# Performance work log

Measured on AMD Instinct MI355X. Metric: run time of the kernel, lower is better.

The kernel has to match this reference:

```python
import jax, jax.numpy as jnp
import numpy as np

BATCH, SEQ, D_MODEL, N_HEADS, D_HEAD = 2, 2048, 2048, 16, 128
ATTN_SCALE = np.sqrt(D_HEAD).astype(np.float32)
IGNORE = jnp.float32(-1e5)


def setup_inputs() -> dict:
    key = jax.random.key(0)
    ks = jax.random.split(key, 5)
    init = 1.0 / np.sqrt(D_MODEL)
    return {
        "x": jax.random.normal(ks[0], (BATCH, SEQ, D_MODEL), jnp.float32),
        "W_Q": jax.random.normal(ks[1], (N_HEADS, D_MODEL, D_HEAD), jnp.float32) * init,
        "W_K": jax.random.normal(ks[2], (N_HEADS, D_MODEL, D_HEAD), jnp.float32) * init,
        "W_V": jax.random.normal(ks[3], (N_HEADS, D_MODEL, D_HEAD), jnp.float32) * init,
        "W_O": jax.random.normal(ks[4], (N_HEADS, D_HEAD, D_MODEL), jnp.float32) * init,
        "b_Q": jnp.zeros((N_HEADS, D_HEAD), jnp.float32),
        "b_K": jnp.zeros((N_HEADS, D_HEAD), jnp.float32),
        "b_V": jnp.zeros((N_HEADS, D_HEAD), jnp.float32),
        "b_O": jnp.zeros((D_MODEL,), jnp.float32),
    }


def reference(x, W_Q, W_K, W_V, W_O, b_Q, b_K, b_V, b_O):
    # q,k,v: [batch, pos, head, d_head]
    q = jnp.einsum('bpd,hde->bphe', x, W_Q) + b_Q
    k = jnp.einsum('bpd,hde->bphe', x, W_K) + b_K
    v = jnp.einsum('bpd,hde->bphe', x, W_V) + b_V
    # scores: [batch, head, query_pos, key_pos]
    scores = jnp.einsum('bqhe,bkhe->bhqk', q, k) / ATTN_SCALE
    S = x.shape[1]
    causal = jnp.tril(jnp.ones((S, S), bool))
    scores = jnp.where(causal, scores, IGNORE)
    attn = jax.nn.softmax(scores, axis=-1)
    z = jnp.einsum('bkhe,bhqk->bqhe', v, attn)
    out = jnp.einsum('bqhe,hed->bqd', z, W_O) + b_O
    return out
```

## Files before the change

kernel.cpp:

```cpp
#include <hip/hip_runtime.h>

typedef unsigned int uint;
typedef unsigned short ushort;
typedef __bf16 bf16x8 __attribute__((ext_vector_type(8)));
typedef float f32x4 __attribute__((ext_vector_type(4)));
typedef uint u32x4 __attribute__((ext_vector_type(4)));

#define DEV static __device__ __forceinline__

#define BATCH 2
#define SEQ 2048
#define DMODEL 2048
#define NHEADS 16
#define DHEAD 128
#define MROWS (BATCH*SEQ)
#define RSCALE 0.08838834764831845f

DEV bf16x8 as_frag(u32x4 v) { return __builtin_bit_cast(bf16x8, v); }
DEV ushort f2bf(float f) {
  uint u = __builtin_bit_cast(uint, f);
  u += 0x7fffu + ((u >> 16) & 1u);
  return (ushort)(u >> 16);
}
DEV u32x4 lds_ld16(const ushort* p) { return *(const u32x4*)p; }

DEV void async_cp16(const ushort* g, ushort* l) {
  __builtin_amdgcn_global_load_lds(
      (const __attribute__((address_space(1))) uint*)g,
      (__attribute__((address_space(3))) uint*)l, 16, 0, 0);
}

__global__ __launch_bounds__(256) void convert_f32_bf16(
    const float* __restrict__ src, ushort* __restrict__ dst, int n4)
{
  int i = blockIdx.x * 256 + threadIdx.x;
  if (i >= n4) return;
  const float4* s4 = (const float4*)src;
  float4 v = s4[i];
  union { ushort u[4]; uint2 w; } o;
  o.u[0] = f2bf(v.x); o.u[1] = f2bf(v.y); o.u[2] = f2bf(v.z); o.u[3] = f2bf(v.w);
  ((uint2*)dst)[i] = o.w;
}

__global__ __launch_bounds__(256) void transpose_f32_bf16(
    const float* __restrict__ src, ushort* __restrict__ dst, int R, int C)
{
  __shared__ ushort t[32][33];
  size_t slice = (size_t)blockIdx.z * R * C;
  src += slice; dst += slice;
  int c0 = blockIdx.x * 32, r0 = blockIdx.y * 32;
  int x = threadIdx.x & 31, y = threadIdx.x >> 5;
  #pragma unroll
  for (int i = 0; i < 32; i += 8)
    t[y + i][x] = f2bf(src[(size_t)(r0 + y + i) * C + (c0 + x)]);
  __syncthreads();
  #pragma unroll
  for (int i = 0; i < 32; i += 8)
    dst[(size_t)(c0 + y + i) * R + (r0 + x)] = t[x][y + i];
}

__global__ __launch_bounds__(256, 3) void gemm_qkv(
    const ushort* __restrict__ xb,
    const ushort* __restrict__ WqT, const ushort* __restrict__ WkT,
    const ushort* __restrict__ WvT,
    const float* __restrict__ bQ, const float* __restrict__ bK,
    const float* __restrict__ bV,
    ushort* __restrict__ Qo, ushort* __restrict__ Ko, ushort* __restrict__ Vt)
{
  int mt = blockIdx.x;
  int h  = blockIdx.y;
  int which = blockIdx.z;
  const ushort* Bt = (which == 0) ? WqT : (which == 1) ? WkT : WvT;
  const float* bias = (which == 0) ? bQ : (which == 1) ? bK : bV;
  Bt += (size_t)h * DHEAD * DMODEL;
  bias += h * DHEAD;

  __shared__ __align__(16) ushort As[128 * 64];
  __shared__ __align__(16) ushort Bs[128 * 64];

  int tid = threadIdx.x, lane = tid & 63, w = tid >> 6;
  int wm = w >> 1, wn = w & 1;
  int l16 = lane & 15, quad = lane >> 4;

  const ushort* Ag = xb + (size_t)(mt * 128) * DMODEL;

  int soff[4]; int sc[4];
  #pragma unroll
  for (int t = 0; t < 4; t++) {
    int c = w * 4 + t;
    int r = c * 8 + (lane >> 3);
    int p = lane & 7;
    int g = p ^ (r & 7);
    soff[t] = r * DMODEL + g * 8;
    sc[t] = c * 512;
  }

  f32x4 acc[4][4] = {};

  for (int k0 = 0; k0 < DMODEL; k0 += 64) {
    __syncthreads();
    #pragma unroll
    for (int t = 0; t < 4; t++) {
      async_cp16(Ag + soff[t] + k0, As + sc[t]);
      async_cp16(Bt + soff[t] + k0, Bs + sc[t]);
    }
    __syncthreads();
    #pragma unroll
    for (int kk = 0; kk < 2; kk++) {
      bf16x8 a[4], b[4];
      #pragma unroll
      for (int i = 0; i < 4; i++) {
        int row = wm * 64 + i * 16 + l16;
        int p = (kk * 4 + quad) ^ (l16 & 7);
        a[i] = as_frag(lds_ld16(As + row * 64 + p * 8));
      }
      #pragma unroll
      for (int i = 0; i < 4; i++) {
        int row = wn * 64 + i * 16 + l16;
        int p = (kk * 4 + quad) ^ (l16 & 7);
        b[i] = as_frag(lds_ld16(Bs + row * 64 + p * 8));
      }
      #pragma unroll
      for (int i = 0; i < 4; i++)
        #pragma unroll
        for (int j = 0; j < 4; j++)
          acc[i][j] = __builtin_amdgcn_mfma_f32_16x16x32_bf16(a[i], b[j], acc[i][j], 0, 0, 0);
    }
  }

  float scale = (which == 0) ? RSCALE : 1.0f;
  #pragma unroll
  for (int i = 0; i < 4; i++) {
    #pragma unroll
    for (int j = 0; j < 4; j++) {
      int col = wn * 64 + j * 16 + l16;
      float bb = bias[col];
      #pragma unroll
      for (int r = 0; r < 4; r++) {
        int row = mt * 128 + wm * 64 + i * 16 + quad * 4 + r;
        int b_ = row >> 11, p = row & 2047;
        int bh = b_ * NHEADS + h;
        ushort val = f2bf((acc[i][j][r] + bb) * scale);
        if (which == 2) {
          Vt[((size_t)bh * DHEAD + col) * SEQ + p] = val;
        } else {
          ushort* Out = (which == 0) ? Qo : Ko;
          Out[((size_t)bh * SEQ + p) * DHEAD + col] = val;
        }
      }
    }
  }
}

__global__ __launch_bounds__(256, 3) void flash_attn(
    const ushort* __restrict__ Q, const ushort* __restrict__ K,
    const ushort* __restrict__ Vt, ushort* __restrict__ Z)
{
  int a  = blockIdx.x;
  int bh = blockIdx.y;
  const ushort* Qg = Q + (size_t)bh * SEQ * DHEAD;
  const ushort* Kg = K + (size_t)bh * SEQ * DHEAD;
  const ushort* Vg = Vt + (size_t)bh * DHEAD * SEQ;

  __shared__ __align__(16) ushort Ks[64 * 128];
  __shared__ __align__(16) ushort Vs[128 * 64];
  __shared__ __align__(16) ushort Ps[64 * 72];

  int tid = threadIdx.x, lane = tid & 63, w = tid >> 6;
  int l16 = lane & 15, quad = lane >> 4;

  int kOff[4], kLds[4], vOff[4], vLds[4];
  #pragma unroll
  for (int t = 0; t < 4; t++) {
    int c = w * 4 + t;
    int rk = c * 4 + (lane >> 4);
    int pk = lane & 15;
    int gk = (pk & 8) | ((pk & 7) ^ (rk & 7));
    kOff[t] = rk * DHEAD + gk * 8;
    kLds[t] = c * 512;
    int ev = c * 8 + (lane >> 3);
    int pv = lane & 7;
    int gv = pv ^ (ev & 7);
    vOff[t] = ev * SEQ + gv * 8;
    vLds[t] = c * 512;
  }

  #pragma unroll
  for (int ph = 0; ph < 2; ph++) {
    int qt = ph ? a : (31 - a);
    int q0 = qt * 64;

    bf16x8 qf[4];
    int qrow = q0 + w * 16 + l16;
    #pragma unroll
    for (int kb = 0; kb < 4; kb++)
      qf[kb] = as_frag(*(const u32x4*)(Qg + qrow * DHEAD + kb * 32 + quad * 8));

    float m_i[4], l_i[4];
    #pragma unroll
    for (int i = 0; i < 4; i++) { m_i[i] = -1e30f; l_i[i] = 0.0f; }
    f32x4 zacc[8] = {};

    for (int j = 0; j <= qt; j++) {
      int k0 = j * 64;
      __syncthreads();
      #pragma unroll
      for (int t = 0; t < 4; t++) {
        async_cp16(Kg + k0 * DHEAD + kOff[t], Ks + kLds[t]);
        async_cp16(Vg + k0 + vOff[t], Vs + vLds[t]);
      }
      __syncthreads();

      f32x4 s[4] = {};
      #pragma unroll
      for (int kb = 0; kb < 4; kb++) {
        #pragma unroll
        for (int n = 0; n < 4; n++) {
          int r = n * 16 + l16;
          int ug = kb * 4 + quad;
          int p = (ug & 8) | ((ug & 7) ^ (r & 7));
          bf16x8 b = as_frag(lds_ld16(Ks + r * 128 + p * 8));
          s[n] = __builtin_amdgcn_mfma_f32_16x16x32_bf16(qf[kb], b, s[n], 0, 0, 0);
        }
      }
      if (j == qt) {
        #pragma unroll
        for (int n = 0; n < 4; n++)
          #pragma unroll
          for (int i = 0; i < 4; i++) {
            int qr = 16 * w + quad * 4 + i;
            int kr = n * 16 + l16;
            if (kr > qr) s[n][i] = -1e30f;
          }
      }
      float mx[4];
      #pragma unroll
      for (int i = 0; i < 4; i++)
        mx[i] = fmaxf(fmaxf(s[0][i], s[1][i]), fmaxf(s[2][i], s[3][i]));
      #pragma unroll
      for (int off = 1; off < 16; off <<= 1)
        #pragma unroll
        for (int i = 0; i < 4; i++)
          mx[i] = fmaxf(mx[i], __shfl_xor(mx[i], off, 64));

      float alpha[4], rsum[4];
      #pragma unroll
      for (int i = 0; i < 4; i++) {
        float mn = fmaxf(m_i[i], mx[i]);
        alpha[i] = __expf(m_i[i] - mn);
        m_i[i] = mn;
        rsum[i] = 0.0f;
      }
      #pragma unroll
      for (int n = 0; n < 4; n++)
        #pragma unroll
        for (int i = 0; i < 4; i++) {
          float p = __expf(s[n][i] - m_i[i]);
          rsum[i] += p;
          int row = 16 * w + quad * 4 + i, col = n * 16 + l16;
          Ps[row * 72 + col] = f2bf(p);
        }
      #pragma unroll
      for (int off = 1; off < 16; off <<= 1)
        #pragma unroll
        for (int i = 0; i < 4; i++)
          rsum[i] += __shfl_xor(rsum[i], off, 64);
      #pragma unroll
      for (int i = 0; i < 4; i++) l_i[i] = l_i[i] * alpha[i] + rsum[i];
      #pragma unroll
      for (int n = 0; n < 8; n++)
        #pragma unroll
        for (int i = 0; i < 4; i++) zacc[n][i] *= alpha[i];

      __syncthreads();

      #pragma unroll
      for (int kk = 0; kk < 2; kk++) {
        bf16x8 af = as_frag(lds_ld16(Ps + (w * 16 + l16) * 72 + (kk * 4 + quad) * 8));
        #pragma unroll
        for (int n = 0; n < 8; n++) {
          int e = n * 16 + l16;
          int ug = kk * 4 + quad;
          int p = ug ^ (e & 7);
          bf16x8 b = as_frag(lds_ld16(Vs + e * 64 + p * 8));
          zacc[n] = __builtin_amdgcn_mfma_f32_16x16x32_bf16(af, b, zacc[n], 0, 0, 0);
        }
      }
    }

    int b_ = bh >> 4, h = bh & 15;
    #pragma unroll
    for (int n = 0; n < 8; n++)
      #pragma unroll
      for (int i = 0; i < 4; i++) {
        int row = q0 + 16 * w + quad * 4 + i;
        int col = h * DHEAD + n * 16 + l16;
        Z[((size_t)(b_ * SEQ + row)) * DMODEL + col] = f2bf(zacc[n][i] / l_i[i]);
      }
  }
}

__global__ __launch_bounds__(256, 3) void gemm_out(
    const ushort* __restrict__ Zin, const ushort* __restrict__ WoT,
    const float* __restrict__ bO, float* __restrict__ out)
{
  int mt = blockIdx.x, ntile = blockIdx.y;
  __shared__ __align__(16) ushort As[128 * 64];
  __shared__ __align__(16) ushort Bs[128 * 64];
  int tid = threadIdx.x, lane = tid & 63, w = tid >> 6;
  int wm = w >> 1, wn = w & 1;
  int l16 = lane & 15, quad = lane >> 4;

  const ushort* Ag = Zin + (size_t)(mt * 128) * DMODEL;
  const ushort* Bg = WoT + (size_t)(ntile * 128) * DMODEL;

  int soff[4]; int sc[4];
  #pragma unroll
  for (int t = 0; t < 4; t++) {
    int c = w * 4 + t;
    int r = c * 8 + (lane >> 3);
    int p = lane & 7;
    int g = p ^ (r & 7);
    soff[t] = r * DMODEL + g * 8;
    sc[t] = c * 512;
  }

  f32x4 acc[4][4] = {};
  for (int k0 = 0; k0 < DMODEL; k0 += 64) {
    __syncthreads();
    #pragma unroll
    for (int t = 0; t < 4; t++) {
      async_cp16(Ag + soff[t] + k0, As + sc[t]);
      async_cp16(Bg + soff[t] + k0, Bs + sc[t]);
    }
    __syncthreads();
    #pragma unroll
    for (int kk = 0; kk < 2; kk++) {
      bf16x8 a[4], b[4];
      #pragma unroll
      for (int i = 0; i < 4; i++) {
        int row = wm * 64 + i * 16 + l16;
        int p = (kk * 4 + quad) ^ (l16 & 7);
        a[i] = as_frag(lds_ld16(As + row * 64 + p * 8));
      }
      #pragma unroll
      for (int i = 0; i < 4; i++) {
        int row = wn * 64 + i * 16 + l16;
        int p = (kk * 4 + quad) ^ (l16 & 7);
        b[i] = as_frag(lds_ld16(Bs + row * 64 + p * 8));
      }
      #pragma unroll
      for (int i = 0; i < 4; i++)
        #pragma unroll
        for (int j = 0; j < 4; j++)
          acc[i][j] = __builtin_amdgcn_mfma_f32_16x16x32_bf16(a[i], b[j], acc[i][j], 0, 0, 0);
    }
  }
  #pragma unroll
  for (int i = 0; i < 4; i++) {
    #pragma unroll
    for (int j = 0; j < 4; j++) {
      int col = ntile * 128 + wn * 64 + j * 16 + l16;
      float bb = bO[col];
      #pragma unroll
      for (int r = 0; r < 4; r++) {
        int row = mt * 128 + wm * 64 + i * 16 + quad * 4 + r;
        out[(size_t)row * DMODEL + col] = acc[i][j][r] + bb;
      }
    }
  }
}

extern "C" void kernel_launch(void* const* d_in, const int* in_sizes, int n_in,
                              void* d_out, int out_size, void* d_ws, size_t ws_size,
                              hipStream_t stream)
{
  const float* x  = (const float*)d_in[0];
  const float* Wq = (const float*)d_in[1];
  const float* Wk = (const float*)d_in[2];
  const float* Wv = (const float*)d_in[3];
  const float* Wo = (const float*)d_in[4];
  const float* bQ = (const float*)d_in[5];
  const float* bK = (const float*)d_in[6];
  const float* bV = (const float*)d_in[7];
  const float* bO = (const float*)d_in[8];
  float* out = (float*)d_out;

  ushort* ws = (ushort*)d_ws;
  const size_t WSZ = (size_t)NHEADS * DHEAD * DMODEL;
  const size_t QSZ = (size_t)BATCH * NHEADS * SEQ * DHEAD;
  ushort* xb  = ws;
  ushort* WqT = xb + (size_t)MROWS * DMODEL;
  ushort* WkT = WqT + WSZ;
  ushort* WvT = WkT + WSZ;
  ushort* WoT = WvT + WSZ;
  ushort* Qb  = WoT + (size_t)DMODEL * DMODEL;
  ushort* Kb  = Qb + QSZ;
  ushort* VtB = Kb + QSZ;
  ushort* Zb  = VtB + QSZ;

  dim3 tb(256);
  convert_f32_bf16<<<dim3(MROWS * DMODEL / 4 / 256), tb, 0, stream>>>(
      x, xb, MROWS * DMODEL / 4);
  transpose_f32_bf16<<<dim3(4, 64, 16), tb, 0, stream>>>(Wq, WqT, DMODEL, DHEAD);
  transpose_f32_bf16<<<dim3(4, 64, 16), tb, 0, stream>>>(Wk, WkT, DMODEL, DHEAD);
  transpose_f32_bf16<<<dim3(4, 64, 16), tb, 0, stream>>>(Wv, WvT, DMODEL, DHEAD);
  transpose_f32_bf16<<<dim3(64, 64, 1), tb, 0, stream>>>(Wo, WoT, DMODEL, DMODEL);

  gemm_qkv<<<dim3(32, 16, 3), tb, 0, stream>>>(xb, WqT, WkT, WvT, bQ, bK, bV,
                                               Qb, Kb, VtB);

  flash_attn<<<dim3(16, 32), tb, 0, stream>>>(Qb, Kb, VtB, Zb);

  gemm_out<<<dim3(32, 16), tb, 0, stream>>>(Zb, WoT, bO, out);
}
```

Baseline: 389.9 us.

## Fuse prep kernels, double-buffer attention K/V tiles, use exp2 softmax

Merges the input convert and four weight-transpose launches into one prep kernel to cut launch overhead. The flash attention K/V tiles are double-buffered, so the next tile's async load overlaps the current tile's compute, and the barriers are rearranged to one per iteration. Softmax now uses a native exp2 with log2(e) folded into the Q scale, and launch-bound occupancy hints are changed on all three GEMM/attention kernels. Double buffering doubles attention LDS use, and the single barrier must still order Ps writes and reads and the buffer reuse correctly.

```diff
diff --git a/kernel.cpp b/kernel.cpp
--- a/kernel.cpp
+++ b/kernel.cpp
@@ -15,6 +15,9 @@
 #define DHEAD 128
 #define MROWS (BATCH*SEQ)
 #define RSCALE 0.08838834764831845f
+#define LOG2E  1.4426950408889634f
+
+DEV float fast_exp2(float x) { return __builtin_amdgcn_exp2f(x); }
 
 DEV bf16x8 as_frag(u32x4 v) { return __builtin_bit_cast(bf16x8, v); }
 DEV ushort f2bf(float f) {
@@ -30,36 +33,53 @@
       (__attribute__((address_space(3))) uint*)l, 16, 0, 0);
 }
 
-__global__ __launch_bounds__(256) void convert_f32_bf16(
-    const float* __restrict__ src, ushort* __restrict__ dst, int n4)
+__global__ __launch_bounds__(256) void prep(
+    const float* __restrict__ x,
+    const float* __restrict__ Wq, const float* __restrict__ Wk,
+    const float* __restrict__ Wv, const float* __restrict__ Wo,
+    ushort* __restrict__ xb, ushort* __restrict__ WqT,
+    ushort* __restrict__ WkT, ushort* __restrict__ WvT,
+    ushort* __restrict__ WoT)
 {
-  int i = blockIdx.x * 256 + threadIdx.x;
-  if (i >= n4) return;
-  const float4* s4 = (const float4*)src;
-  float4 v = s4[i];
-  union { ushort u[4]; uint2 w; } o;
-  o.u[0] = f2bf(v.x); o.u[1] = f2bf(v.y); o.u[2] = f2bf(v.z); o.u[3] = f2bf(v.w);
-  ((uint2*)dst)[i] = o.w;
-}
-
-__global__ __launch_bounds__(256) void transpose_f32_bf16(
-    const float* __restrict__ src, ushort* __restrict__ dst, int R, int C)
-{
+  int id = blockIdx.x;
+  if (id < 8192) {
+    int i = id * 256 + threadIdx.x;
+    float4 v = ((const float4*)x)[i];
+    union { ushort u[4]; uint2 w; } o;
+    o.u[0] = f2bf(v.x); o.u[1] = f2bf(v.y); o.u[2] = f2bf(v.z); o.u[3] = f2bf(v.w);
+    ((uint2*)xb)[i] = o.w;
+    return;
+  }
   __shared__ ushort t[32][33];
-  size_t slice = (size_t)blockIdx.z * R * C;
-  src += slice; dst += slice;
-  int c0 = blockIdx.x * 32, r0 = blockIdx.y * 32;
-  int x = threadIdx.x & 31, y = threadIdx.x >> 5;
+  id -= 8192;
+  const float* src; ushort* dst; int R, C, c0, r0;
+  if (id < 12288) {
+    int which = id >> 12;
+    int r = id & 4095;
+    int slice = r >> 8;
+    int rem = r & 255;
+    int ty = rem >> 2, tx = rem & 3;
+    const float* S[3] = {Wq, Wk, Wv};
+    ushort* D[3] = {WqT, WkT, WvT};
+    src = S[which] + (size_t)slice * DMODEL * DHEAD;
+    dst = D[which] + (size_t)slice * DMODEL * DHEAD;
+    R = DMODEL; C = DHEAD; c0 = tx * 32; r0 = ty * 32;
+  } else {
+    id -= 12288;
+    int tx = id & 63, ty = id >> 6;
+    src = Wo; dst = WoT; R = DMODEL; C = DMODEL; c0 = tx * 32; r0 = ty * 32;
+  }
+  int xx = threadIdx.x & 31, yy = threadIdx.x >> 5;
   #pragma unroll
   for (int i = 0; i < 32; i += 8)
-    t[y + i][x] = f2bf(src[(size_t)(r0 + y + i) * C + (c0 + x)]);
+    t[yy + i][xx] = f2bf(src[(size_t)(r0 + yy + i) * C + (c0 + xx)]);
   __syncthreads();
   #pragma unroll
   for (int i = 0; i < 32; i += 8)
-    dst[(size_t)(c0 + y + i) * R + (r0 + x)] = t[x][y + i];
-}
-
-__global__ __launch_bounds__(256, 3) void gemm_qkv(
+    dst[(size_t)(c0 + yy + i) * R + (r0 + xx)] = t[xx][yy + i];
+}
+
+__global__ __launch_bounds__(256, 4) void gemm_qkv(
     const ushort* __restrict__ xb,
     const ushort* __restrict__ WqT, const ushort* __restrict__ WkT,
     const ushort* __restrict__ WvT,
@@ -128,7 +148,7 @@
     }
   }
 
-  float scale = (which == 0) ? RSCALE : 1.0f;
+  float scale = (which == 0) ? RSCALE * LOG2E : 1.0f;
   #pragma unroll
   for (int i = 0; i < 4; i++) {
     #pragma unroll
@@ -152,7 +172,7 @@
   }
 }
 
-__global__ __launch_bounds__(256, 3) void flash_attn(
+__global__ __launch_bounds__(256, 2) void flash_attn(
     const ushort* __restrict__ Q, const ushort* __restrict__ K,
     const ushort* __restrict__ Vt, ushort* __restrict__ Z)
 {
@@ -162,27 +182,26 @@
   const ushort* Kg = K + (size_t)bh * SEQ * DHEAD;
   const ushort* Vg = Vt + (size_t)bh * DHEAD * SEQ;
 
-  __shared__ __align__(16) ushort Ks[64 * 128];
-  __shared__ __align__(16) ushort Vs[128 * 64];
+  __shared__ __align__(16) ushort Ks[2][64 * 128];
+  __shared__ __align__(16) ushort Vs[2][128 * 64];
   __shared__ __align__(16) ushort Ps[64 * 72];
 
   int tid = threadIdx.x, lane = tid & 63, w = tid >> 6;
   int l16 = lane & 15, quad = lane >> 4;
 
-  int kOff[4], kLds[4], vOff[4], vLds[4];
+  int kOff[4], vOff[4], cLds[4];
   #pragma unroll
   for (int t = 0; t < 4; t++) {
     int c = w * 4 + t;
+    cLds[t] = c * 512;
     int rk = c * 4 + (lane >> 4);
     int pk = lane & 15;
     int gk = (pk & 8) | ((pk & 7) ^ (rk & 7));
     kOff[t] = rk * DHEAD + gk * 8;
-    kLds[t] = c * 512;
     int ev = c * 8 + (lane >> 3);
     int pv = lane & 7;
     int gv = pv ^ (ev & 7);
     vOff[t] = ev * SEQ + gv * 8;
-    vLds[t] = c * 512;
   }
 
   #pragma unroll
@@ -201,15 +220,25 @@
     for (int i = 0; i < 4; i++) { m_i[i] = -1e30f; l_i[i] = 0.0f; }
     f32x4 zacc[8] = {};
 
+    #pragma unroll
+    for (int t = 0; t < 4; t++) {
+      async_cp16(Kg + kOff[t], Ks[0] + cLds[t]);
+      async_cp16(Vg + vOff[t], Vs[0] + cLds[t]);
+    }
+    __syncthreads();
+
     for (int j = 0; j <= qt; j++) {
-      int k0 = j * 64;
-      __syncthreads();
-      #pragma unroll
-      for (int t = 0; t < 4; t++) {
-        async_cp16(Kg + k0 * DHEAD + kOff[t], Ks + kLds[t]);
-        async_cp16(Vg + k0 + vOff[t], Vs + vLds[t]);
-      }
-      __syncthreads();
+      int cur = j & 1;
+      if (j < qt) {
+        int k1 = (j + 1) * 64;
+        #pragma unroll
+        for (int t = 0; t < 4; t++) {
+          async_cp16(Kg + k1 * DHEAD + kOff[t], Ks[cur ^ 1] + cLds[t]);
+          async_cp16(Vg + k1 + vOff[t], Vs[cur ^ 1] + cLds[t]);
+        }
+      }
+      const ushort* KsC = Ks[cur];
+      const ushort* VsC = Vs[cur];
 
       f32x4 s[4] = {};
       #pragma unroll
@@ -219,7 +248,7 @@
           int r = n * 16 + l16;
           int ug = kb * 4 + quad;
           int p = (ug & 8) | ((ug & 7) ^ (r & 7));
-          bf16x8 b = as_frag(lds_ld16(Ks + r * 128 + p * 8));
+          bf16x8 b = as_frag(lds_ld16(KsC + r * 128 + p * 8));
           s[n] = __builtin_amdgcn_mfma_f32_16x16x32_bf16(qf[kb], b, s[n], 0, 0, 0);
         }
       }
@@ -247,7 +276,7 @@
       #pragma unroll
       for (int i = 0; i < 4; i++) {
         float mn = fmaxf(m_i[i], mx[i]);
-        alpha[i] = __expf(m_i[i] - mn);
+        alpha[i] = fast_exp2(m_i[i] - mn);
         m_i[i] = mn;
         rsum[i] = 0.0f;
       }
@@ -255,7 +284,7 @@
       for (int n = 0; n < 4; n++)
         #pragma unroll
         for (int i = 0; i < 4; i++) {
-          float p = __expf(s[n][i] - m_i[i]);
+          float p = fast_exp2(s[n][i] - m_i[i]);
           rsum[i] += p;
           int row = 16 * w + quad * 4 + i, col = n * 16 + l16;
           Ps[row * 72 + col] = f2bf(p);
@@ -272,8 +301,6 @@
         #pragma unroll
         for (int i = 0; i < 4; i++) zacc[n][i] *= alpha[i];
 
-      __syncthreads();
-
       #pragma unroll
       for (int kk = 0; kk < 2; kk++) {
         bf16x8 af = as_frag(lds_ld16(Ps + (w * 16 + l16) * 72 + (kk * 4 + quad) * 8));
@@ -282,10 +309,11 @@
           int e = n * 16 + l16;
           int ug = kk * 4 + quad;
           int p = ug ^ (e & 7);
-          bf16x8 b = as_frag(lds_ld16(Vs + e * 64 + p * 8));
+          bf16x8 b = as_frag(lds_ld16(VsC + e * 64 + p * 8));
           zacc[n] = __builtin_amdgcn_mfma_f32_16x16x32_bf16(af, b, zacc[n], 0, 0, 0);
         }
       }
+      __syncthreads();
     }
 
     int b_ = bh >> 4, h = bh & 15;
@@ -300,7 +328,7 @@
   }
 }
 
-__global__ __launch_bounds__(256, 3) void gemm_out(
+__global__ __launch_bounds__(256, 4) void gemm_out(
     const ushort* __restrict__ Zin, const ushort* __restrict__ WoT,
     const float* __restrict__ bO, float* __restrict__ out)
 {
@@ -400,12 +428,8 @@
   ushort* Zb  = VtB + QSZ;
 
   dim3 tb(256);
-  convert_f32_bf16<<<dim3(MROWS * DMODEL / 4 / 256), tb, 0, stream>>>(
-      x, xb, MROWS * DMODEL / 4);
-  transpose_f32_bf16<<<dim3(4, 64, 16), tb, 0, stream>>>(Wq, WqT, DMODEL, DHEAD);
-  transpose_f32_bf16<<<dim3(4, 64, 16), tb, 0, stream>>>(Wk, WkT, DMODEL, DHEAD);
-  transpose_f32_bf16<<<dim3(4, 64, 16), tb, 0, stream>>>(Wv, WvT, DMODEL, DHEAD);
-  transpose_f32_bf16<<<dim3(64, 64, 1), tb, 0, stream>>>(Wo, WoT, DMODEL, DMODEL);
+  prep<<<dim3(24576), tb, 0, stream>>>(x, Wq, Wk, Wv, Wo,
+                                       xb, WqT, WkT, WvT, WoT);
 
   gemm_qkv<<<dim3(32, 16, 3), tb, 0, stream>>>(xb, WqT, WkT, WvT, bQ, bK, bV,
                                                Qb, Kb, VtB);
```

Result: faster. 374.1 us (-4.1%).
